# Kernel tuning notes

Measured on AMD Instinct MI355X. Metric: run time of the kernel, lower is better.

Reference implementation:

```python
import jax, jax.numpy as jnp
import numpy as np

DIM = 1024
H = 16
HD = DIM // H  # 64
BASE = 10000.0


def _rope_tables(seq_len, d):
    # freqs over half-dim, then TILED (repeat) along last axis as in the torch code
    freqs = 1.0 / (BASE ** (jnp.arange(0, d, 2, dtype=jnp.float32) / d))  # [d/2]
    t = jnp.arange(seq_len, dtype=jnp.float32)
    f = jnp.outer(t, freqs)  # [S, d/2]
    cos = jnp.concatenate([jnp.cos(f), jnp.cos(f)], axis=-1)  # [S, d] (tiled, NOT interleaved)
    sin = jnp.concatenate([jnp.sin(f), jnp.sin(f)], axis=-1)
    return cos, sin


def _apply_rope(x):
    # x: [B, H, S, d]; rotation pairs adjacent elements (2i, 2i+1)
    S, d = x.shape[-2], x.shape[-1]
    cos, sin = _rope_tables(S, d)  # [S, d]
    xh = x.reshape(*x.shape[:-1], d // 2, 2)
    x_rot = jnp.stack([-xh[..., 1], xh[..., 0]], axis=-1).reshape(x.shape)
    return x * cos + x_rot * sin


def setup_inputs() -> dict:
    key = jax.random.key(0)
    ks = jax.random.split(key, 7)
    B, Sq, Sk = 16, 512, 512
    s = 0.02
    return {
        "x": jax.random.normal(ks[0], (B, Sq, DIM), jnp.float32),
        "context": jax.random.normal(ks[1], (B, Sk, DIM), jnp.float32),
        "Wq": jax.random.normal(ks[2], (DIM, DIM), jnp.float32) * s,
        "Wk": jax.random.normal(ks[3], (DIM, DIM), jnp.float32) * s,
        "Wv": jax.random.normal(ks[4], (DIM, DIM), jnp.float32) * s,
        "Wo": jax.random.normal(ks[5], (DIM, DIM), jnp.float32) * s,
        "bo": jax.random.normal(ks[6], (DIM,), jnp.float32) * s,
    }


def reference(x, context, Wq, Wk, Wv, Wo, bo):
    B, Sq, _ = x.shape
    Sk = context.shape[1]
    scale = HD ** -0.5
    # projections, split heads: [B, H, S, HD]
    q = (x @ Wq).reshape(B, Sq, H, HD).transpose(0, 2, 1, 3)
    k = (context @ Wk).reshape(B, Sk, H, HD).transpose(0, 2, 1, 3)
    v = (context @ Wv).reshape(B, Sk, H, HD).transpose(0, 2, 1, 3)
    q = _apply_rope(q)
    k = _apply_rope(k)
    attn = jax.nn.softmax(jnp.einsum("bhqd,bhkd->bhqk", q, k) * scale, axis=-1)
    out = jnp.einsum("bhqk,bhkd->bhqd", attn, v)
    out = out.transpose(0, 2, 1, 3).reshape(B, Sq, DIM)
    return out @ Wo + bo  # dropout is identity (p=0 / eval)
```

## Files before the change

kernel.cpp:

```cpp
#include <hip/hip_runtime.h>

#define DIM   1024
#define NH    16
#define HD    64
#define BATCH 16
#define SEQ   512
#define MROWS (BATCH*SEQ)
#define SL2E  0.18033688011112042f

typedef __bf16 bf16x8 __attribute__((ext_vector_type(8)));
typedef float  floatx4 __attribute__((ext_vector_type(4)));
typedef short  short4v __attribute__((ext_vector_type(4)));

static __device__ __forceinline__ unsigned short f2bf(float f) {
    union { float f; unsigned u; } v; v.f = f;
    return (unsigned short)((v.u + 0x8000u) >> 16);
}
static __device__ __forceinline__ unsigned pk2(float a, float b) {
    union { float f; unsigned u; } x, y; x.f = a; y.f = b;
    return ((x.u + 0x8000u) >> 16) | ((y.u + 0x8000u) & 0xffff0000u);
}

static __device__ __forceinline__ void glds16(const void* g, void* l) {
    __builtin_amdgcn_global_load_lds(
        (const __attribute__((address_space(1))) unsigned int*)g,
        (__attribute__((address_space(3))) unsigned int*)l, 16, 0, 0);
}

__global__ __launch_bounds__(256)
void prep(const float* __restrict__ x, const float* __restrict__ ctx,
          const float* __restrict__ Wq, const float* __restrict__ Wk,
          const float* __restrict__ Wv, const float* __restrict__ Wo,
          unsigned short* __restrict__ xb, unsigned short* __restrict__ cb,
          unsigned short* __restrict__ WqT, unsigned short* __restrict__ WkT,
          unsigned short* __restrict__ WvT, unsigned short* __restrict__ WoT,
          float2* __restrict__ cstab)
{
    __shared__ float tile[32][33];
    const int blk = blockIdx.x, t = threadIdx.x;
    if (blk < 8192) {
        const float* src = (blk < 4096) ? x : ctx;
        unsigned short* dst = (blk < 4096) ? xb : cb;
        int e = ((blk & 4095) * 256 + t) * 8;
        float4 f0 = *(const float4*)&src[e];
        float4 f1 = *(const float4*)&src[e + 4];
        uint4 o = { pk2(f0.x, f0.y), pk2(f0.z, f0.w), pk2(f1.x, f1.y), pk2(f1.z, f1.w) };
        *(uint4*)&dst[e] = o;
    } else if (blk < 12288) {
        int id2 = blk - 8192;
        const float* W; unsigned short* T;
        switch (id2 >> 10) {
            case 0:  W = Wq; T = WqT; break;
            case 1:  W = Wk; T = WkT; break;
            case 2:  W = Wv; T = WvT; break;
            default: W = Wo; T = WoT; break;
        }
        int local = id2 & 1023;
        int n0 = (local & 31) * 32, k0 = (local >> 5) * 32;
        int tx = t & 31, ty = t >> 5;
        #pragma unroll
        for (int a = 0; a < 4; a++)
            tile[ty + 8 * a][tx] = W[(size_t)(k0 + ty + 8 * a) * DIM + n0 + tx];
        __syncthreads();
        #pragma unroll
        for (int a = 0; a < 4; a++)
            T[(size_t)(n0 + ty + 8 * a) * DIM + k0 + tx] = f2bf(tile[tx][ty + 8 * a]);
    } else {
        int gid = (blk - 12288) * 256 + t;
        int d = gid & (HD - 1), s = gid >> 6;
        const float C = -0.41524101186092f;
        float f = exp2f((float)(d & 31) * C);
        float a = (float)s * f;
        cstab[gid] = make_float2(cosf(a), sinf(a));
    }
}

static __device__ __forceinline__ void gemm_main(
    const unsigned short* __restrict__ A, const unsigned short* __restrict__ Bt,
    int m0, int n0, unsigned short* As, unsigned short* Bs, floatx4 acc[4][4])
{
    const int t = threadIdx.x;
    const int w = t >> 6, l = t & 63;
    const int wm = w >> 1, wn = w & 1;
    const int lane16 = l & 15, quad = l >> 4;
    const int lr = l >> 3;
    const int gsw = ((l & 7) ^ lr) * 8;
    const int co0 = (quad ^ (lane16 & 7)) * 8;
    const int co1 = co0 ^ 32;

    #pragma unroll
    for (int mi = 0; mi < 4; mi++)
        #pragma unroll
        for (int ni = 0; ni < 4; ni++) acc[mi][ni] = (floatx4){0.f, 0.f, 0.f, 0.f};

    const unsigned short* ap = A  + (size_t)(m0 + w * 32 + lr) * DIM + gsw;
    const unsigned short* bp = Bt + (size_t)(n0 + w * 32 + lr) * DIM + gsw;

    for (int kt = 0; kt < DIM; kt += 64) {
        #pragma unroll
        for (int j = 0; j < 4; j++) {
            glds16(ap + (size_t)j * 8 * DIM + kt, &As[(w * 4 + j) * 512]);
            glds16(bp + (size_t)j * 8 * DIM + kt, &Bs[(w * 4 + j) * 512]);
        }
        __syncthreads();
        #pragma unroll
        for (int kk = 0; kk < 2; kk++) {
            const int co = kk ? co1 : co0;
            bf16x8 af[4], bfr[4];
            #pragma unroll
            for (int mi = 0; mi < 4; mi++)
                af[mi] = *(const bf16x8*)&As[(wm * 64 + mi * 16 + lane16) * 64 + co];
            #pragma unroll
            for (int ni = 0; ni < 4; ni++)
                bfr[ni] = *(const bf16x8*)&Bs[(wn * 64 + ni * 16 + lane16) * 64 + co];
            #pragma unroll
            for (int mi = 0; mi < 4; mi++)
                #pragma unroll
                for (int ni = 0; ni < 4; ni++)
                    acc[mi][ni] = __builtin_amdgcn_mfma_f32_16x16x32_bf16(bfr[ni], af[mi], acc[mi][ni], 0, 0, 0);
        }
        __syncthreads();
    }
}

static __device__ __forceinline__ void proj_epilogue(
    unsigned short* __restrict__ Out, const float2* __restrict__ cstab,
    int m0, int n0, int mode, floatx4 acc[4][4])
{
    const int t = threadIdx.x;
    const int w = t >> 6, l = t & 63;
    const int wm = w >> 1, wn = w & 1;
    const int lane16 = l & 15, quad = l >> 4;

    if (mode == 0) {
        #pragma unroll
        for (int mi = 0; mi < 4; mi++) {
            int m = m0 + wm * 64 + mi * 16 + lane16;
            int s = m & 511, b = m >> 9;
            #pragma unroll
            for (int ni = 0; ni < 4; ni++) {
                int n = n0 + wn * 64 + ni * 16 + quad * 4;
                int h = n >> 6, d0 = n & 63;
                const float4* cp = (const float4*)&cstab[s * HD + d0];
                float4 c01 = cp[0];
                float4 c23 = cp[1];
                floatx4 v = acc[mi][ni];
                float r0 = v[0] * c01.x - v[1] * c01.y;
                float r1 = fmaf(v[0], c01.w, v[1] * c01.z);
                float r2 = v[2] * c23.x - v[3] * c23.y;
                float r3 = fmaf(v[2], c23.w, v[3] * c23.z);
                uint2 o = { pk2(r0, r1), pk2(r2, r3) };
                *(uint2*)&Out[((size_t)(b * NH + h) * SEQ + s) * HD + d0] = o;
            }
        }
    } else {
        #pragma unroll
        for (int mi = 0; mi < 4; mi++) {
            int m = m0 + wm * 64 + mi * 16 + lane16;
            #pragma unroll
            for (int ni = 0; ni < 4; ni++) {
                int n = n0 + wn * 64 + ni * 16 + quad * 4;
                floatx4 v = acc[mi][ni];
                uint2 o = { pk2(v[0], v[1]), pk2(v[2], v[3]) };
                *(uint2*)&Out[((size_t)(n >> 9) * DIM + m) * SEQ + (n & 511)] = o;
            }
        }
    }
}

__global__ __launch_bounds__(256)
void proj_kv(const unsigned short* __restrict__ cb,
             const unsigned short* __restrict__ WkT, const unsigned short* __restrict__ WvT,
             unsigned short* __restrict__ Kb, unsigned short* __restrict__ Vtb,
             const float2* __restrict__ cstab)
{
    __shared__ unsigned short As[128 * 64];
    __shared__ unsigned short Bs[128 * 64];
    const int id = blockIdx.x;
    const int local = id & 511;
    const int xcd = local & 7, seq = local >> 3;
    const unsigned short *A, *Bt; unsigned short* Out;
    int m0, n0, mode;
    if (id < 512) { A = cb;  Bt = WkT; Out = Kb;  mode = 0;
                    n0 = (seq & 7) * 128; m0 = (xcd + 8 * (seq >> 3)) * 128; }
    else          { A = WvT; Bt = cb;  Out = Vtb; mode = 1;
                    m0 = (seq & 7) * 128; n0 = (xcd + 8 * (seq >> 3)) * 128; }
    floatx4 acc[4][4];
    gemm_main(A, Bt, m0, n0, As, Bs, acc);
    proj_epilogue(Out, cstab, m0, n0, mode, acc);
}

__global__ __launch_bounds__(256)
void proj_q(const unsigned short* __restrict__ xb, const unsigned short* __restrict__ WqT,
            unsigned short* __restrict__ Qb, const float2* __restrict__ cstab)
{
    __shared__ unsigned short As[128 * 64];
    __shared__ unsigned short Bs[128 * 64];
    const int id = blockIdx.x;
    const int xcd = id & 7, seq = id >> 3;
    const int n0 = (seq & 7) * 128, m0 = (xcd + 8 * (seq >> 3)) * 128;
    floatx4 acc[4][4];
    gemm_main(xb, WqT, m0, n0, As, Bs, acc);
    proj_epilogue(Qb, cstab, m0, n0, 0, acc);
}

__global__ __launch_bounds__(256)
void out_gemm(const unsigned short* __restrict__ Ab, const unsigned short* __restrict__ WoT,
              float* __restrict__ O, const float* __restrict__ bias)
{
    __shared__ unsigned short As[64 * 64];
    __shared__ unsigned short Bs[128 * 64];
    const int id = blockIdx.x;
    const int xcd = id & 7, seq = id >> 3;
    const int n0 = (seq & 7) * 128;
    const int m0 = (xcd + 8 * (seq >> 3)) * 64;

    const int t = threadIdx.x;
    const int w = t >> 6, l = t & 63;
    const int wm = w >> 1, wn = w & 1;
    const int lane16 = l & 15, quad = l >> 4;
    const int lr = l >> 3;
    const int gsw = ((l & 7) ^ lr) * 8;
    const int co0 = (quad ^ (lane16 & 7)) * 8;
    const int co1 = co0 ^ 32;

    floatx4 acc[2][4];
    #pragma unroll
    for (int mi = 0; mi < 2; mi++)
        #pragma unroll
        for (int ni = 0; ni < 4; ni++) acc[mi][ni] = (floatx4){0.f, 0.f, 0.f, 0.f};

    const unsigned short* ap = Ab  + (size_t)(m0 + w * 16 + lr) * DIM + gsw;
    const unsigned short* bp = WoT + (size_t)(n0 + w * 32 + lr) * DIM + gsw;

    for (int kt = 0; kt < DIM; kt += 64) {
        #pragma unroll
        for (int j = 0; j < 2; j++)
            glds16(ap + (size_t)j * 8 * DIM + kt, &As[(w * 2 + j) * 512]);
        #pragma unroll
        for (int j = 0; j < 4; j++)
            glds16(bp + (size_t)j * 8 * DIM + kt, &Bs[(w * 4 + j) * 512]);
        __syncthreads();
        #pragma unroll
        for (int kk = 0; kk < 2; kk++) {
            const int co = kk ? co1 : co0;
            bf16x8 af[2], bfr[4];
            #pragma unroll
            for (int mi = 0; mi < 2; mi++)
                af[mi] = *(const bf16x8*)&As[(wm * 32 + mi * 16 + lane16) * 64 + co];
            #pragma unroll
            for (int ni = 0; ni < 4; ni++)
                bfr[ni] = *(const bf16x8*)&Bs[(wn * 64 + ni * 16 + lane16) * 64 + co];
            #pragma unroll
            for (int mi = 0; mi < 2; mi++)
                #pragma unroll
                for (int ni = 0; ni < 4; ni++)
                    acc[mi][ni] = __builtin_amdgcn_mfma_f32_16x16x32_bf16(bfr[ni], af[mi], acc[mi][ni], 0, 0, 0);
        }
        __syncthreads();
    }

    #pragma unroll
    for (int ni = 0; ni < 4; ni++) {
        int n = n0 + wn * 64 + ni * 16 + quad * 4;
        float4 bv = *(const float4*)&bias[n];
        #pragma unroll
        for (int mi = 0; mi < 2; mi++) {
            int m = m0 + wm * 32 + mi * 16 + lane16;
            floatx4 v = acc[mi][ni];
            float4 o = { v[0] + bv.x, v[1] + bv.y, v[2] + bv.z, v[3] + bv.w };
            *(float4*)&O[(size_t)m * DIM + n] = o;
        }
    }
}

__global__ __launch_bounds__(256, 4)
void attn_v4(const unsigned short* __restrict__ Q, const unsigned short* __restrict__ K,
             const unsigned short* __restrict__ Vt, unsigned short* __restrict__ Out)
{
    __shared__ unsigned short Ks[2][64][72];
    __shared__ unsigned short Vts[2][64][72];

    const int id = blockIdx.x;
    const int qi = (id >> 3) & 3;
    const int bh = (id & 7) | ((id >> 5) << 3);
    const int q0 = qi * 128;
    const int t  = threadIdx.x;
    const int w = t >> 6, l = t & 63;
    const int lane16 = l & 15, quad = l >> 4;
    const size_t base = (size_t)bh * SEQ * HD;

    bf16x8 qreg[2][2];
    #pragma unroll
    for (int st = 0; st < 2; st++)
        #pragma unroll
        for (int kk = 0; kk < 2; kk++)
            qreg[st][kk] = *(const bf16x8*)&Q[base +
                (size_t)(q0 + st * 64 + w * 16 + lane16) * HD + kk * 32 + quad * 8];

    const int sr = t >> 3, sc = (t & 7) * 8;
    const unsigned short* kp0 = K  + base + (size_t)sr * HD + sc;
    const unsigned short* kp1 = kp0 + (size_t)32 * HD;
    const unsigned short* vp0 = Vt + base + (size_t)sr * SEQ + sc;
    const unsigned short* vp1 = vp0 + (size_t)32 * SEQ;

    uint4 kr0 = *(const uint4*)kp0;  kp0 += (size_t)64 * HD;
    uint4 kr1 = *(const uint4*)kp1;  kp1 += (size_t)64 * HD;
    uint4 vr0 = *(const uint4*)vp0;  vp0 += 64;
    uint4 vr1 = *(const uint4*)vp1;  vp1 += 64;

    floatx4 acc_o[2][4];
    float lsum[2] = {0.f, 0.f};
    #pragma unroll
    for (int st = 0; st < 2; st++)
        #pragma unroll
        for (int dt = 0; dt < 4; dt++) acc_o[st][dt] = (floatx4){0.f, 0.f, 0.f, 0.f};

    for (int it = 0; it < 8; ++it) {
        const int cb = it & 1;
        *(uint4*)&Ks[cb][sr][sc]       = kr0;
        *(uint4*)&Ks[cb][sr + 32][sc]  = kr1;
        *(uint4*)&Vts[cb][sr][sc]      = vr0;
        *(uint4*)&Vts[cb][sr + 32][sc] = vr1;
        if (it < 7) {
            kr0 = *(const uint4*)kp0;  kp0 += (size_t)64 * HD;
            kr1 = *(const uint4*)kp1;  kp1 += (size_t)64 * HD;
            vr0 = *(const uint4*)vp0;  vp0 += 64;
            vr1 = *(const uint4*)vp1;  vp1 += 64;
        }
        asm volatile("s_waitcnt lgkmcnt(0)" ::: "memory");
        __builtin_amdgcn_s_barrier();

        short4v pa[2][4];
        #pragma unroll
        for (int st = 0; st < 2; st++) {
            floatx4 sacc[4];
            #pragma unroll
            for (int c = 0; c < 4; c++) sacc[c] = (floatx4){0.f, 0.f, 0.f, 0.f};
            #pragma unroll
            for (int kk = 0; kk < 2; kk++)
                #pragma unroll
                for (int c = 0; c < 4; c++) {
                    bf16x8 kf = *(const bf16x8*)&Ks[cb][c * 16 + lane16][kk * 32 + quad * 8];
                    sacc[c] = __builtin_amdgcn_mfma_f32_16x16x32_bf16(kf, qreg[st][kk], sacc[c], 0, 0, 0);
                }
            #pragma unroll
            for (int c = 0; c < 4; c++) {
                short4v pk;
                #pragma unroll
                for (int i = 0; i < 4; i++) {
                    float pv = exp2f(sacc[c][i] * SL2E);
                    lsum[st] += pv;
                    pk[i] = (short)f2bf(pv);
                }
                pa[st][c] = pk;
            }
        }
        #pragma unroll
        for (int c = 0; c < 4; c++) {
            #pragma unroll
            for (int dt = 0; dt < 4; dt++) {
                short4v vf = *(const short4v*)&Vts[cb][dt * 16 + lane16][c * 16 + quad * 4];
                #pragma unroll
                for (int st = 0; st < 2; st++)
                    acc_o[st][dt] = __builtin_amdgcn_mfma_f32_16x16x16bf16_1k(
                        vf, pa[st][c], acc_o[st][dt], 0, 0, 0);
            }
        }
    }

    const int b = bh >> 4, h = bh & 15;
    #pragma unroll
    for (int st = 0; st < 2; st++) {
        float rs = lsum[st];
        rs += __shfl_xor(rs, 16, 64);
        rs += __shfl_xor(rs, 32, 64);
        float inv = 1.0f / rs;
        int s = q0 + st * 64 + w * 16 + lane16;
        size_t rowbase = (size_t)(b * SEQ + s) * DIM + h * HD;
        #pragma unroll
        for (int dt = 0; dt < 4; dt++) {
            floatx4 v = acc_o[st][dt];
            uint2 o = { pk2(v[0] * inv, v[1] * inv), pk2(v[2] * inv, v[3] * inv) };
            *(uint2*)&Out[rowbase + dt * 16 + quad * 4] = o;
        }
    }
}

extern "C" void kernel_launch(void* const* d_in, const int* in_sizes, int n_in,
                              void* d_out, int out_size, void* d_ws, size_t ws_size,
                              hipStream_t stream)
{
    const float* x   = (const float*)d_in[0];
    const float* ctx = (const float*)d_in[1];
    const float* Wq  = (const float*)d_in[2];
    const float* Wk  = (const float*)d_in[3];
    const float* Wv  = (const float*)d_in[4];
    const float* Wo  = (const float*)d_in[5];
    const float* bo  = (const float*)d_in[6];

    const size_t NW = (size_t)DIM * DIM;
    const size_t NB = (size_t)MROWS * DIM;

    unsigned short* x_bf   = (unsigned short*)d_ws;
    unsigned short* ctx_bf = x_bf + NB;
    unsigned short* WqT    = ctx_bf + NB;
    unsigned short* WkT    = WqT + NW;
    unsigned short* WvT    = WkT + NW;
    unsigned short* WoT    = WvT + NW;
    unsigned short* Kb     = WoT + NW;
    unsigned short* Vtb    = Kb + NB;
    float2*         cstab  = (float2*)(Vtb + NB);
    unsigned short* Qb     = (unsigned short*)d_out;
    unsigned short* Ab     = x_bf;

    prep<<<12416, 256, 0, stream>>>(x, ctx, Wq, Wk, Wv, Wo,
                                    x_bf, ctx_bf, WqT, WkT, WvT, WoT, cstab);

    proj_kv<<<1024, 256, 0, stream>>>(ctx_bf, WkT, WvT, Kb, Vtb, cstab);

    proj_q<<<512, 256, 0, stream>>>(x_bf, WqT, Qb, cstab);

    attn_v4<<<1024, 256, 0, stream>>>(Qb, Kb, Vtb, Ab);

    out_gemm<<<1024, 256, 0, stream>>>(Ab, WoT, (float*)d_out, bo);
}
```

Baseline: 268.3 us.

## Merge Q/K/V projections into one launch and enlarge out_gemm tiles

The separate proj_q kernel is folded into the K/V projection kernel as a third 512-block segment, so one 1536-block launch replaces two. The output GEMM moves from 64x128 tiles with 256 threads to 128x128 tiles with 512 threads (8 waves), halving its block count. This aims to cut a launch and the tail between launches, and to raise operand reuse in the output projection. The trade-off is a larger LDS footprint per block, which may reduce occupancy.

```diff
diff --git a/kernel.cpp b/kernel.cpp
--- a/kernel.cpp
+++ b/kernel.cpp
@@ -169,51 +169,39 @@
 }
 
 __global__ __launch_bounds__(256)
-void proj_kv(const unsigned short* __restrict__ cb,
-             const unsigned short* __restrict__ WkT, const unsigned short* __restrict__ WvT,
-             unsigned short* __restrict__ Kb, unsigned short* __restrict__ Vtb,
-             const float2* __restrict__ cstab)
+void proj_qkv(const unsigned short* __restrict__ xb, const unsigned short* __restrict__ cb,
+              const unsigned short* __restrict__ WqT, const unsigned short* __restrict__ WkT,
+              const unsigned short* __restrict__ WvT,
+              unsigned short* __restrict__ Qb, unsigned short* __restrict__ Kb,
+              unsigned short* __restrict__ Vtb, const float2* __restrict__ cstab)
 {
     __shared__ unsigned short As[128 * 64];
     __shared__ unsigned short Bs[128 * 64];
     const int id = blockIdx.x;
-    const int local = id & 511;
+    const int seg = id >> 9, local = id & 511;
     const int xcd = local & 7, seq = local >> 3;
     const unsigned short *A, *Bt; unsigned short* Out;
     int m0, n0, mode;
-    if (id < 512) { A = cb;  Bt = WkT; Out = Kb;  mode = 0;
-                    n0 = (seq & 7) * 128; m0 = (xcd + 8 * (seq >> 3)) * 128; }
-    else          { A = WvT; Bt = cb;  Out = Vtb; mode = 1;
-                    m0 = (seq & 7) * 128; n0 = (xcd + 8 * (seq >> 3)) * 128; }
+    if (seg == 0)      { A = cb;  Bt = WkT; Out = Kb;  mode = 0;
+                         n0 = (seq & 7) * 128; m0 = (xcd + 8 * (seq >> 3)) * 128; }
+    else if (seg == 1) { A = WvT; Bt = cb;  Out = Vtb; mode = 1;
+                         m0 = (seq & 7) * 128; n0 = (xcd + 8 * (seq >> 3)) * 128; }
+    else               { A = xb;  Bt = WqT; Out = Qb;  mode = 0;
+                         n0 = (seq & 7) * 128; m0 = (xcd + 8 * (seq >> 3)) * 128; }
     floatx4 acc[4][4];
     gemm_main(A, Bt, m0, n0, As, Bs, acc);
     proj_epilogue(Out, cstab, m0, n0, mode, acc);
 }
 
-__global__ __launch_bounds__(256)
-void proj_q(const unsigned short* __restrict__ xb, const unsigned short* __restrict__ WqT,
-            unsigned short* __restrict__ Qb, const float2* __restrict__ cstab)
+__global__ __launch_bounds__(512)
+void out_gemm(const unsigned short* __restrict__ Ab, const unsigned short* __restrict__ WoT,
+              float* __restrict__ O, const float* __restrict__ bias)
 {
     __shared__ unsigned short As[128 * 64];
     __shared__ unsigned short Bs[128 * 64];
     const int id = blockIdx.x;
     const int xcd = id & 7, seq = id >> 3;
     const int n0 = (seq & 7) * 128, m0 = (xcd + 8 * (seq >> 3)) * 128;
-    floatx4 acc[4][4];
-    gemm_main(xb, WqT, m0, n0, As, Bs, acc);
-    proj_epilogue(Qb, cstab, m0, n0, 0, acc);
-}
-
-__global__ __launch_bounds__(256)
-void out_gemm(const unsigned short* __restrict__ Ab, const unsigned short* __restrict__ WoT,
-              float* __restrict__ O, const float* __restrict__ bias)
-{
-    __shared__ unsigned short As[64 * 64];
-    __shared__ unsigned short Bs[128 * 64];
-    const int id = blockIdx.x;
-    const int xcd = id & 7, seq = id >> 3;
-    const int n0 = (seq & 7) * 128;
-    const int m0 = (xcd + 8 * (seq >> 3)) * 64;
 
     const int t = threadIdx.x;
     const int w = t >> 6, l = t & 63;
@@ -231,15 +219,14 @@
         for (int ni = 0; ni < 4; ni++) acc[mi][ni] = (floatx4){0.f, 0.f, 0.f, 0.f};
 
     const unsigned short* ap = Ab  + (size_t)(m0 + w * 16 + lr) * DIM + gsw;
-    const unsigned short* bp = WoT + (size_t)(n0 + w * 32 + lr) * DIM + gsw;
+    const unsigned short* bp = WoT + (size_t)(n0 + w * 16 + lr) * DIM + gsw;
 
     for (int kt = 0; kt < DIM; kt += 64) {
         #pragma unroll
-        for (int j = 0; j < 2; j++)
+        for (int j = 0; j < 2; j++) {
             glds16(ap + (size_t)j * 8 * DIM + kt, &As[(w * 2 + j) * 512]);
-        #pragma unroll
-        for (int j = 0; j < 4; j++)
-            glds16(bp + (size_t)j * 8 * DIM + kt, &Bs[(w * 4 + j) * 512]);
+            glds16(bp + (size_t)j * 8 * DIM + kt, &Bs[(w * 2 + j) * 512]);
+        }
         __syncthreads();
         #pragma unroll
         for (int kk = 0; kk < 2; kk++) {
@@ -417,11 +404,10 @@
     prep<<<12416, 256, 0, stream>>>(x, ctx, Wq, Wk, Wv, Wo,
                                     x_bf, ctx_bf, WqT, WkT, WvT, WoT, cstab);
 
-    proj_kv<<<1024, 256, 0, stream>>>(ctx_bf, WkT, WvT, Kb, Vtb, cstab);
-
-    proj_q<<<512, 256, 0, stream>>>(x_bf, WqT, Qb, cstab);
+    proj_qkv<<<1536, 256, 0, stream>>>(x_bf, ctx_bf, WqT, WkT, WvT,
+                                       Qb, Kb, Vtb, cstab);
 
     attn_v4<<<1024, 256, 0, stream>>>(Qb, Kb, Vtb, Ab);
 
-    out_gemm<<<1024, 256, 0, stream>>>(Ab, WoT, (float*)d_out, bo);
-}
+    out_gemm<<<512, 512, 0, stream>>>(Ab, WoT, (float*)d_out, bo);
+}
```

Result: faster. 256.6 us (-4.4%).
